# Kernel tuning notes

Measured on AMD Instinct MI355X. Metric: run time of the kernel, lower is better.

The kernel has to match this reference:

```python
import jax, jax.numpy as jnp
import numpy as np

B, S, V, D = 64, 24, 50257, 300
N, E, Ln, Le = 256, 1024, 4, 4
HL = 512               # LSTM hidden size
HEADS, HD = 4, 128
OUT = HEADS * HD       # 512, GAT out dim (concat heads)
NA = 3000              # num answers


def setup_inputs() -> dict:
    key = jax.random.key(0)
    ks = jax.random.split(key, 24)
    s = 0.02
    inp = {}
    inp["question"] = jax.random.randint(ks[0], (B, S), 0, V)
    inp["question_mask"] = jnp.ones((B, S), dtype=jnp.int32)
    inp["node_tokens"] = jax.random.randint(ks[1], (B, N, Ln), 0, V)
    inp["edge_tokens"] = jax.random.randint(ks[2], (B, E, Le), 0, V)
    inp["src_ids"] = jax.random.randint(ks[3], (B, E), 0, N)
    inp["dst_ids"] = jax.random.randint(ks[4], (B, E), 0, N)
    inp["word_emb"] = jax.random.normal(ks[5], (V, D)) * s
    inp["W_ih"] = jax.random.normal(ks[6], (D, 4 * HL)) * s
    inp["W_hh"] = jax.random.normal(ks[7], (HL, 4 * HL)) * s
    inp["b_lstm"] = jnp.zeros((4 * HL,))
    inp["W_node"] = jax.random.normal(ks[8], (D, HEADS * HD)) * s
    inp["W_rel"] = jax.random.normal(ks[9], (D, HEADS * HD)) * s
    inp["a_src"] = jax.random.normal(ks[10], (HEADS, HD)) * s
    inp["a_dst"] = jax.random.normal(ks[11], (HEADS, HD)) * s
    inp["a_edge"] = jax.random.normal(ks[12], (HEADS, HD)) * s
    inp["W_edge_upd"] = jax.random.normal(ks[13], (D, D)) * s
    inp["W_qnode"] = jax.random.normal(ks[14], (HL, OUT)) * s
    inp["b_qnode"] = jnp.zeros((OUT,))
    inp["W_qedge"] = jax.random.normal(ks[15], (HL, D)) * s
    inp["b_qedge"] = jnp.zeros((D,))
    inp["W_edge_prj"] = jax.random.normal(ks[16], (D, OUT)) * s
    inp["b_edge_prj"] = jnp.zeros((OUT,))
    inp["W_mid"] = jax.random.normal(ks[17], (2 * OUT, 3 * OUT)) * s
    inp["b_mid"] = jnp.zeros((3 * OUT,))
    inp["W_pre"] = jax.random.normal(ks[18], (3 * OUT, NA)) * s
    inp["b_pre"] = jnp.zeros((NA,))
    return inp


def _lstm_last_hidden(x, mask, W_ih, W_hh, b):
    # x: [B,S,D], mask: [B,S] -> last valid hidden state [B,HL]
    h0 = jnp.zeros((x.shape[0], HL), x.dtype)
    def step(carry, t):
        h, c = carry
        xt, mt = t
        g = xt @ W_ih + h @ W_hh + b
        i, f, gg, o = jnp.split(g, 4, axis=-1)
        c_new = jax.nn.sigmoid(f) * c + jax.nn.sigmoid(i) * jnp.tanh(gg)
        h_new = jax.nn.sigmoid(o) * jnp.tanh(c_new)
        m = (mt > 0)[:, None]
        return (jnp.where(m, h_new, h), jnp.where(m, c_new, c)), None
    (h, _), _ = jax.lax.scan(step, (h0, h0), (x.transpose(1, 0, 2), mask.T))
    return h


def reference(question, question_mask, node_tokens, edge_tokens, src_ids, dst_ids,
              word_emb, W_ih, W_hh, b_lstm, W_node, W_rel, a_src, a_dst, a_edge,
              W_edge_upd, W_qnode, b_qnode, W_qedge, b_qedge, W_edge_prj, b_edge_prj,
              W_mid, b_mid, W_pre, b_pre):
    # language encoder
    seq = word_emb[question]                               # [B,S,D]
    q_emb = _lstm_last_hidden(seq, question_mask, W_ih, W_hh, b_lstm)  # [B,HL]
    # graph features: sum word embeddings of node/edge phrases (get_graph_feat)
    nf = word_emb[node_tokens].sum(2).reshape(B * N, D)    # [BN,D]
    ef = word_emb[edge_tokens].sum(2).reshape(B * E, D)    # [BE,D]
    # batched graph with global node ids
    offs = (jnp.arange(B) * N)[:, None]
    src = (src_ids + offs).reshape(-1)
    dst = (dst_ids + offs).reshape(-1)
    # multi-head GAT with edge (relation) features
    h = (nf @ W_node).reshape(B * N, HEADS, HD)
    r = (ef @ W_rel).reshape(B * E, HEADS, HD)
    logits = jax.nn.leaky_relu(
        (h[src] * a_src).sum(-1) + (h[dst] * a_dst).sum(-1) + (r * a_edge).sum(-1),
        negative_slope=0.2)                                # [BE,HEADS]
    mx = jax.ops.segment_max(logits, dst, num_segments=B * N)
    ex = jnp.exp(logits - mx[dst])
    den = jax.ops.segment_sum(ex, dst, num_segments=B * N)
    alpha = ex / (den[dst] + 1e-9)
    node_out = jax.ops.segment_sum(alpha[..., None] * (h[src] + r), dst,
                                   num_segments=B * N)
    node_out = jax.nn.elu(node_out).reshape(B, N, OUT)     # ndata['feat']
    edge_out = jax.nn.relu(ef @ W_edge_upd).reshape(B, E, D)  # edata['feat']
    # per-graph readout (dgl.unbatch + torch.sum loop == segment sum over graphs)
    nodes = node_out.sum(1)                                # [B,OUT]
    edges = edge_out.sum(1)                                # [B,D]
    # question projections + fusion
    question_edges = (q_emb @ W_qedge + b_qedge) + edges
    question_nodes = (q_emb @ W_qnode + b_qnode) + nodes
    q_edges = question_edges @ W_edge_prj + b_edge_prj
    q = jnp.concatenate([q_edges, question_nodes], axis=1)  # [B,2*OUT]
    mid = q @ W_mid + b_mid
    return mid @ W_pre + b_pre                              # [B,NA]
```

## Files before the change

### kernel.cpp

```cpp
#include <hip/hip_runtime.h>
#include <hip/hip_bf16.h>
#include <cstdint>
#include <cstddef>

typedef unsigned short u16;
typedef __attribute__((ext_vector_type(8))) short bf16x8;
typedef __attribute__((ext_vector_type(4))) float f32x4;

#define BB   64
#define SS   24
#define DD   300
#define DP   304
#define HLS  512
#define BNN  16384
#define BEE  65536
#define NAA  3000

static constexpr size_t O_COUNTS = 0;
static constexpr size_t O_FILL   = 65536;
static constexpr size_t O_ESUM   = 131072;
static constexpr size_t O_H0     = 207872;
static constexpr size_t O_C      = 338944;
static constexpr size_t Z_BYTES  = 470016;
static constexpr size_t O_H1     = 470016;
static constexpr size_t O_XPROJ  = 601088;
static constexpr size_t O_BT_NODE = O_XPROJ;
static constexpr size_t O_BT_REL  = O_XPROJ + 311296;
static constexpr size_t O_BT_EDGE = O_XPROJ + 622592;
static constexpr size_t O_NF     = 13184000;
static constexpr size_t O_EF     = 23145472;
static constexpr size_t O_HFEAT  = 62991360;
static constexpr size_t O_RFEAT  = 79768576;
static constexpr size_t O_SSRC   = 146877440;
static constexpr size_t O_SDST   = 147139584;
static constexpr size_t O_SE     = 147401728;
static constexpr size_t O_SG     = 148450304;
static constexpr size_t O_DG     = 148712448;
static constexpr size_t O_RS     = 148974592;
static constexpr size_t O_ELIST  = 149040128;
static constexpr size_t O_LG     = 149302272;
static constexpr size_t O_NOUT   = 150350848;
static constexpr size_t O_NSUM   = 167128064;
static constexpr size_t O_QN     = 167259136;
static constexpr size_t O_QE     = 167390208;
static constexpr size_t O_QCAT   = 167467008;
static constexpr size_t O_MID    = 167729152;

__device__ __forceinline__ float bf(u16 u) {
  union { unsigned int i; float f; } c; c.i = ((unsigned int)u) << 16; return c.f;
}
__device__ __forceinline__ u16 f2bu(float f) {
  union { float f; unsigned int i; } c; c.f = f;
  unsigned int r = c.i + 0x7fffu + ((c.i >> 16) & 1u);
  return (u16)(r >> 16);
}

__global__ __launch_bounds__(256) void k_zero(float* __restrict__ p, int n) {
  int i = blockIdx.x * 256 + threadIdx.x, st = gridDim.x * 256;
  for (; i < n; i += st) p[i] = 0.f;
}

__global__ __launch_bounds__(256) void k_binit(const float* __restrict__ bias,
    const float* __restrict__ extra, float* __restrict__ out, int N, int ldo, int lde) {
  int col = blockIdx.x * 256 + threadIdx.x;
  int b = blockIdx.y;
  if (col < N) {
    float v = bias ? bias[col] : 0.f;
    if (extra) v += extra[(size_t)b * lde + col];
    out[(size_t)b * ldo + col] = v;
  }
}

__global__ __launch_bounds__(256) void k_feat(const int* __restrict__ toks, const float* __restrict__ emb,
                                              u16* __restrict__ outp) {
  int tid = threadIdx.x;
  int r = blockIdx.x * 4 + (tid >> 6);
  int lane = tid & 63;
  int t0 = toks[r * 4 + 0], t1 = toks[r * 4 + 1], t2 = toks[r * 4 + 2], t3 = toks[r * 4 + 3];
  const float* e0 = emb + (size_t)t0 * DD;
  const float* e1 = emb + (size_t)t1 * DD;
  const float* e2 = emb + (size_t)t2 * DD;
  const float* e3 = emb + (size_t)t3 * DD;
#pragma unroll
  for (int p = 0; p < 2; ++p) {
    int c = p * 256 + lane * 4;
    if (c >= DP) continue;
    ushort4 o;
    if (c + 3 < DD) {
      float4 a = *(const float4*)&e0[c], b4 = *(const float4*)&e1[c];
      float4 d = *(const float4*)&e2[c], e = *(const float4*)&e3[c];
      o.x = f2bu(a.x + b4.x + d.x + e.x);
      o.y = f2bu(a.y + b4.y + d.y + e.y);
      o.z = f2bu(a.z + b4.z + d.z + e.z);
      o.w = f2bu(a.w + b4.w + d.w + e.w);
    } else {
      o.x = o.y = o.z = o.w = 0;
    }
    *(ushort4*)&outp[(size_t)r * DP + c] = o;
  }
}

__global__ __launch_bounds__(256) void k_trans(const float* __restrict__ W, int N, int Npad,
                                               u16* __restrict__ Wt) {
  __shared__ float t[32][33];
  int tx = threadIdx.x & 31;
  int ty = threadIdx.x >> 5;
  int c0 = blockIdx.x * 32;
  int k0 = blockIdx.y * 32;
#pragma unroll
  for (int r = 0; r < 4; ++r) {
    int k = k0 + ty + r * 8;
    int c = c0 + tx;
    t[ty + r * 8][tx] = (k < DD && c < N) ? W[(size_t)k * N + c] : 0.f;
  }
  __syncthreads();
#pragma unroll
  for (int r = 0; r < 4; ++r) {
    int c = c0 + ty + r * 8;
    int k = k0 + tx;
    if (c < Npad && k < DP) Wt[(size_t)c * DP + k] = f2bu(t[tx][ty + r * 8]);
  }
}

__global__ __launch_bounds__(256) void gemm_f32(
    const float* __restrict__ A, int lda, const int* __restrict__ rowmap,
    const float* __restrict__ W, int N, int K, float* __restrict__ Cf) {
  __shared__ float As[32][128];
  __shared__ float Ws[32][128];
  int tid = threadIdx.x;
  int tx = tid & 15, ty = tid >> 4;
  int row0 = blockIdx.y * 128, col0 = blockIdx.x * 128;
  float acc[8][8];
#pragma unroll
  for (int i = 0; i < 8; ++i)
#pragma unroll
    for (int j = 0; j < 8; ++j) acc[i][j] = 0.f;
  for (int k0 = 0; k0 < K; k0 += 32) {
    for (int s = tid; s < 1024; s += 256) {
      int r = s >> 3, kc = (s & 7) << 2, kk = k0 + kc;
      float4 v = {0.f, 0.f, 0.f, 0.f};
      if (kk + 3 < K) {
        int ar = row0 + r;
        if (rowmap) ar = rowmap[ar];
        v = *(const float4*)&A[(size_t)ar * lda + kk];
      } else if (kk < K) {
        int ar = row0 + r;
        if (rowmap) ar = rowmap[ar];
        v.x = A[(size_t)ar * lda + kk];
        if (kk + 1 < K) v.y = A[(size_t)ar * lda + kk + 1];
        if (kk + 2 < K) v.z = A[(size_t)ar * lda + kk + 2];
      }
      As[kc + 0][r] = v.x; As[kc + 1][r] = v.y; As[kc + 2][r] = v.z; As[kc + 3][r] = v.w;
    }
    for (int s = tid; s < 1024; s += 256) {
      int kr = s >> 5, nc = (s & 31) << 2, kk = k0 + kr, col = col0 + nc;
      float4 wv = {0.f, 0.f, 0.f, 0.f};
      if (kk < K && col + 3 < N) wv = *(const float4*)&W[(size_t)kk * N + col];
      *(float4*)&Ws[kr][nc] = wv;
    }
    __syncthreads();
#pragma unroll 8
    for (int k = 0; k < 32; ++k) {
      float a[8], b[8];
      *(float4*)&a[0] = *(float4*)&As[k][ty * 8];
      *(float4*)&a[4] = *(float4*)&As[k][ty * 8 + 4];
      *(float4*)&b[0] = *(float4*)&Ws[k][tx * 8];
      *(float4*)&b[4] = *(float4*)&Ws[k][tx * 8 + 4];
#pragma unroll
      for (int i = 0; i < 8; ++i)
#pragma unroll
        for (int j = 0; j < 8; ++j) acc[i][j] = fmaf(a[i], b[j], acc[i][j]);
    }
    __syncthreads();
  }
#pragma unroll
  for (int i = 0; i < 8; ++i) {
    int gr = row0 + ty * 8 + i;
#pragma unroll
    for (int j = 0; j < 8; ++j) {
      int gc = col0 + tx * 8 + j;
      if (gc < N) Cf[(size_t)gr * N + gc] = acc[i][j];
    }
  }
}

__global__ __launch_bounds__(256) void gemm_mfma(
    const u16* __restrict__ A, const u16* __restrict__ Bt, int N,
    u16* __restrict__ Cb, float* __restrict__ bsum, int mode) {
  __shared__ __align__(16) u16 As[128][40];
  __shared__ __align__(16) u16 Bs[128][40];
  int tid = threadIdx.x;
  int wave = tid >> 6, lane = tid & 63;
  int wr = wave >> 1, wc = wave & 1;
  int row0 = blockIdx.y * 128, col0 = blockIdx.x * 128;
  f32x4 acc[4][4];
#pragma unroll
  for (int i = 0; i < 4; ++i)
#pragma unroll
    for (int j = 0; j < 4; ++j) acc[i][j] = (f32x4){0.f, 0.f, 0.f, 0.f};

  for (int k0 = 0; k0 < DP; k0 += 32) {
    for (int s = tid; s < 1024; s += 256) {
      int r = s >> 3, kc = (s & 7) << 2, kk = k0 + kc;
      ushort4 va = {0, 0, 0, 0}, vb = {0, 0, 0, 0};
      if (kk < DP) {
        va = *(const ushort4*)&A[(size_t)(row0 + r) * DP + kk];
        vb = *(const ushort4*)&Bt[(size_t)(col0 + r) * DP + kk];
      }
      *(ushort4*)&As[r][kc] = va;
      *(ushort4*)&Bs[r][kc] = vb;
    }
    __syncthreads();
    bf16x8 af[4], bfr[4];
    int kb = (lane >> 4) * 8;
    int rl = lane & 15;
#pragma unroll
    for (int i = 0; i < 4; ++i) {
      af[i]  = *(const bf16x8*)&As[wr * 64 + i * 16 + rl][kb];
      bfr[i] = *(const bf16x8*)&Bs[wc * 64 + i * 16 + rl][kb];
    }
#pragma unroll
    for (int i = 0; i < 4; ++i)
#pragma unroll
      for (int j = 0; j < 4; ++j)
        acc[i][j] = __builtin_amdgcn_mfma_f32_16x16x32_bf16(af[i], bfr[j], acc[i][j], 0, 0, 0);
    __syncthreads();
  }

  int g = lane >> 4, rl = lane & 15;
  if (mode == 0) {
#pragma unroll
    for (int i = 0; i < 4; ++i)
#pragma unroll
      for (int j = 0; j < 4; ++j) {
        int gc = col0 + wc * 64 + j * 16 + rl;
#pragma unroll
        for (int reg = 0; reg < 4; ++reg) {
          int gr = row0 + wr * 64 + i * 16 + g * 4 + reg;
          if (gc < N) Cb[(size_t)gr * N + gc] = f2bu(acc[i][j][reg]);
        }
      }
  } else {
    float* red = (float*)&As[0][0];
    __syncthreads();
#pragma unroll
    for (int j = 0; j < 4; ++j) {
      float s = 0.f;
#pragma unroll
      for (int i = 0; i < 4; ++i)
#pragma unroll
        for (int reg = 0; reg < 4; ++reg) s += fmaxf(acc[i][j][reg], 0.f);
      red[(wr * 4 + g) * 128 + wc * 64 + j * 16 + rl] = s;
    }
    __syncthreads();
    if (tid < 128) {
      float s = 0.f;
#pragma unroll
      for (int y = 0; y < 8; ++y) s += red[y * 128 + tid];
      int gc = col0 + tid;
      if (gc < N) atomicAdd(&bsum[(size_t)(row0 >> 10) * N + gc], s);
    }
  }
}

__global__ __launch_bounds__(256) void gemm_small(
    const float* __restrict__ A, int lda, const float* __restrict__ W,
    int N, int K, int ldo, float* __restrict__ out) {
  __shared__ float As[64][256];
  int tid = threadIdx.x;
  int k0 = blockIdx.y * 256;
  int kt = min(256, K - k0);
  int col = blockIdx.x * 64 + (tid & 63);
  int bg = tid >> 6;
  int nseg = kt >> 2;
  for (int s = tid; s < 64 * nseg; s += 256) {
    int r = s / nseg, kq = s - r * nseg;
    *(float4*)&As[r][kq << 2] = *(const float4*)&A[(size_t)r * lda + k0 + (kq << 2)];
  }
  __syncthreads();
  float acc[16];
#pragma unroll
  for (int i = 0; i < 16; ++i) acc[i] = 0.f;
  if (col < N) {
    for (int k = 0; k < kt; k += 4) {
      float w0 = W[(size_t)(k0 + k) * N + col];
      float w1 = W[(size_t)(k0 + k + 1) * N + col];
      float w2 = W[(size_t)(k0 + k + 2) * N + col];
      float w3 = W[(size_t)(k0 + k + 3) * N + col];
#pragma unroll
      for (int bi = 0; bi < 16; ++bi) {
        float4 a4 = *(const float4*)&As[bg * 16 + bi][k];
        acc[bi] = fmaf(a4.x, w0, fmaf(a4.y, w1, fmaf(a4.z, w2, fmaf(a4.w, w3, acc[bi]))));
      }
    }
#pragma unroll
    for (int bi = 0; bi < 16; ++bi)
      atomicAdd(&out[(size_t)(bg * 16 + bi) * ldo + col], acc[bi]);
  }
}

__global__ __launch_bounds__(256) void k_lstm(
    const float* __restrict__ whh, const float* __restrict__ xproj,
    const float* __restrict__ bls, const int* __restrict__ qmask,
    const float* __restrict__ h_in, float* __restrict__ h_out, float* __restrict__ c, int t) {
  __shared__ float hs[4][512];
  int tid = threadIdx.x;
  int j = (blockIdx.x << 6) + (tid & 63);
  int bq = tid >> 6;
  int b = (blockIdx.y << 2) + bq;
  for (int i = tid; i < 2048; i += 256)
    hs[i >> 9][i & 511] = h_in[(size_t)((blockIdx.y << 2) + (i >> 9)) * 512 + (i & 511)];
  __syncthreads();
  float a0 = 0.f, a1 = 0.f, a2 = 0.f, a3 = 0.f;
#pragma unroll 8
  for (int k = 0; k < 512; ++k) {
    float hv = hs[bq][k];
    const float* w = whh + (size_t)k * 2048 + j;
    a0 = fmaf(hv, w[0], a0);
    a1 = fmaf(hv, w[512], a1);
    a2 = fmaf(hv, w[1024], a2);
    a3 = fmaf(hv, w[1536], a3);
  }
  size_t xb = ((size_t)b * SS + t) * 2048;
  float gi = a0 + xproj[xb + j] + bls[j];
  float gf = a1 + xproj[xb + 512 + j] + bls[512 + j];
  float gg = a2 + xproj[xb + 1024 + j] + bls[1024 + j];
  float go = a3 + xproj[xb + 1536 + j] + bls[1536 + j];
  float si = 1.f / (1.f + __expf(-gi));
  float sf = 1.f / (1.f + __expf(-gf));
  float so = 1.f / (1.f + __expf(-go));
  float tg = 2.f / (1.f + __expf(-2.f * gg)) - 1.f;
  int idx = b * 512 + j;
  float cold = c[idx];
  float cn = sf * cold + si * tg;
  float hn = so * (2.f / (1.f + __expf(-2.f * cn)) - 1.f);
  if (qmask[b * SS + t] > 0) { c[idx] = cn; h_out[idx] = hn; }
  else h_out[idx] = h_in[idx];
}

__global__ __launch_bounds__(256) void k_snode(const u16* __restrict__ hfeat,
    const float* __restrict__ a_src, const float* __restrict__ a_dst,
    float* __restrict__ ssrc, float* __restrict__ sdst) {
  __shared__ float as[4 * 132], ad[4 * 132];
  int tid = threadIdx.x;
  for (int i = tid; i < 512; i += 256) {
    int h = i >> 7, d = i & 127;
    as[h * 132 + d] = a_src[i];
    ad[h * 132 + d] = a_dst[i];
  }
  __syncthreads();
  int id = blockIdx.x * 256 + tid;
  int n = id >> 2, h = id & 3;
  const u16* hp = hfeat + (size_t)n * 512 + h * 128;
  float s1 = 0.f, s2 = 0.f;
  for (int d = 0; d < 128; d += 4) {
    ushort4 v = *(const ushort4*)&hp[d];
    float f0 = bf(v.x), f1 = bf(v.y), f2 = bf(v.z), f3 = bf(v.w);
    int o = h * 132 + d;
    s1 += f0 * as[o] + f1 * as[o + 1] + f2 * as[o + 2] + f3 * as[o + 3];
    s2 += f0 * ad[o] + f1 * ad[o + 1] + f2 * ad[o + 2] + f3 * ad[o + 3];
  }
  ssrc[id] = s1; sdst[id] = s2;
}

__global__ __launch_bounds__(256) void k_sedge(const u16* __restrict__ rfeat,
    const float* __restrict__ a_edge, float* __restrict__ se) {
  __shared__ float ae[4 * 132];
  int tid = threadIdx.x;
  for (int i = tid; i < 512; i += 256) { int h = i >> 7, d = i & 127; ae[h * 132 + d] = a_edge[i]; }
  __syncthreads();
  int id = blockIdx.x * 256 + tid;
  int e = id >> 2, h = id & 3;
  const u16* rp = rfeat + (size_t)e * 512 + h * 128;
  float s = 0.f;
  for (int d = 0; d < 128; d += 4) {
    ushort4 v = *(const ushort4*)&rp[d];
    int o = h * 132 + d;
    s += bf(v.x) * ae[o] + bf(v.y) * ae[o + 1] + bf(v.z) * ae[o + 2] + bf(v.w) * ae[o + 3];
  }
  se[id] = s;
}

__global__ __launch_bounds__(256) void k_prep(const int* __restrict__ src, const int* __restrict__ dst,
    int* __restrict__ sg, int* __restrict__ dg, int* __restrict__ counts) {
  int i = blockIdx.x * 256 + threadIdx.x;
  int b = i >> 10;
  sg[i] = (b << 8) + src[i];
  int dgl = (b << 8) + dst[i];
  dg[i] = dgl;
  atomicAdd(&counts[dgl], 1);
}

__global__ __launch_bounds__(256) void k_scan(const int* __restrict__ counts, int* __restrict__ rs) {
  __shared__ int sc[256];
  int b = blockIdx.x, tid = threadIdx.x;
  int v = counts[b * 256 + tid];
  sc[tid] = v;
  __syncthreads();
  for (int off = 1; off < 256; off <<= 1) {
    int add = (tid >= off) ? sc[tid - off] : 0;
    __syncthreads();
    sc[tid] += add;
    __syncthreads();
  }
  rs[b * 256 + tid] = b * 1024 + sc[tid] - v;
}

__global__ __launch_bounds__(256) void k_scatter(const int* __restrict__ dg, const int* __restrict__ rs,
    int* __restrict__ fill, int* __restrict__ elist) {
  int i = blockIdx.x * 256 + threadIdx.x;
  int d = dg[i];
  int pos = rs[d] + atomicAdd(&fill[d], 1);
  elist[pos] = i;
}

__global__ __launch_bounds__(256) void k_logit(const int* __restrict__ sg, const int* __restrict__ dg,
    const float* __restrict__ ssrc, const float* __restrict__ sdst,
    const float* __restrict__ se, float* __restrict__ lg) {
  int i = blockIdx.x * 256 + threadIdx.x;
  int e = i >> 2, h = i & 3;
  float x = ssrc[sg[e] * 4 + h] + sdst[dg[e] * 4 + h] + se[i];
  lg[i] = x > 0.f ? x : 0.2f * x;
}

__global__ __launch_bounds__(256) void k_soft(const int* __restrict__ counts, const int* __restrict__ rs,
    const int* __restrict__ elist, float* __restrict__ lg) {
  int id = blockIdx.x * 256 + threadIdx.x;
  int n = id >> 2, h = id & 3;
  int deg = counts[n];
  if (deg == 0) return;
  int st = rs[n];
  float m = -1e30f;
  for (int i = 0; i < deg; ++i) { int e = elist[st + i]; m = fmaxf(m, lg[e * 4 + h]); }
  float s = 0.f;
  for (int i = 0; i < deg; ++i) {
    int e = elist[st + i];
    float p = __expf(lg[e * 4 + h] - m);
    lg[e * 4 + h] = p;
    s += p;
  }
  float inv = 1.f / (s + 1e-9f);
  for (int i = 0; i < deg; ++i) { int e = elist[st + i]; lg[e * 4 + h] *= inv; }
}

__global__ __launch_bounds__(256) void k_agg(const int* __restrict__ counts, const int* __restrict__ rs,
    const int* __restrict__ elist, const int* __restrict__ sg, const float* __restrict__ lg,
    const u16* __restrict__ hfeat, const u16* __restrict__ rfeat, u16* __restrict__ nout) {
  int n = blockIdx.x;
  int deg = counts[n], st = rs[n];
  int c1 = threadIdx.x, c2 = threadIdx.x + 256;
  float a1 = 0.f, a2 = 0.f;
  for (int i = 0; i < deg; ++i) {
    int e = elist[st + i];
    int s = sg[e];
    float al1 = lg[e * 4 + (c1 >> 7)], al2 = lg[e * 4 + (c2 >> 7)];
    a1 += al1 * (bf(hfeat[(size_t)s * 512 + c1]) + bf(rfeat[(size_t)e * 512 + c1]));
    a2 += al2 * (bf(hfeat[(size_t)s * 512 + c2]) + bf(rfeat[(size_t)e * 512 + c2]));
  }
  a1 = a1 > 0.f ? a1 : __expf(a1) - 1.f;
  a2 = a2 > 0.f ? a2 : __expf(a2) - 1.f;
  nout[(size_t)n * 512 + c1] = f2bu(a1);
  nout[(size_t)n * 512 + c2] = f2bu(a2);
}

__global__ __launch_bounds__(512) void k_nodesum(const u16* __restrict__ nout, float* __restrict__ nsum) {
  int b = blockIdx.x, col = threadIdx.x;
  float s = 0.f;
  for (int n = 0; n < 256; ++n) s += bf(nout[(size_t)((b << 8) + n) * 512 + col]);
  nsum[b * 512 + col] = s;
}

extern "C" void kernel_launch(void* const* d_in, const int* in_sizes, int n_in,
                              void* d_out, int out_size, void* d_ws, size_t ws_size,
                              hipStream_t stream) {
  const int*   question   = (const int*)d_in[0];
  const int*   qmask      = (const int*)d_in[1];
  const int*   node_toks  = (const int*)d_in[2];
  const int*   edge_toks  = (const int*)d_in[3];
  const int*   src_ids    = (const int*)d_in[4];
  const int*   dst_ids    = (const int*)d_in[5];
  const float* word_emb   = (const float*)d_in[6];
  const float* W_ih       = (const float*)d_in[7];
  const float* W_hh       = (const float*)d_in[8];
  const float* b_lstm     = (const float*)d_in[9];
  const float* W_node     = (const float*)d_in[10];
  const float* W_rel      = (const float*)d_in[11];
  const float* a_src      = (const float*)d_in[12];
  const float* a_dst      = (const float*)d_in[13];
  const float* a_edge     = (const float*)d_in[14];
  const float* W_edge_upd = (const float*)d_in[15];
  const float* W_qnode    = (const float*)d_in[16];
  const float* b_qnode    = (const float*)d_in[17];
  const float* W_qedge    = (const float*)d_in[18];
  const float* b_qedge    = (const float*)d_in[19];
  const float* W_edge_prj = (const float*)d_in[20];
  const float* b_edge_prj = (const float*)d_in[21];
  const float* W_mid      = (const float*)d_in[22];
  const float* b_mid      = (const float*)d_in[23];
  const float* W_pre      = (const float*)d_in[24];
  const float* b_pre      = (const float*)d_in[25];
  float* outp = (float*)d_out;

  char* ws = (char*)d_ws;
  int*   counts = (int*)(ws + O_COUNTS);
  int*   fill   = (int*)(ws + O_FILL);
  float* esum   = (float*)(ws + O_ESUM);
  float* h0     = (float*)(ws + O_H0);
  float* cst    = (float*)(ws + O_C);
  float* h1     = (float*)(ws + O_H1);
  float* xproj  = (float*)(ws + O_XPROJ);
  u16*   btn    = (u16*)(ws + O_BT_NODE);
  u16*   btr    = (u16*)(ws + O_BT_REL);
  u16*   bte    = (u16*)(ws + O_BT_EDGE);
  u16*   nf     = (u16*)(ws + O_NF);
  u16*   ef     = (u16*)(ws + O_EF);
  u16*   hfeat  = (u16*)(ws + O_HFEAT);
  u16*   rfeat  = (u16*)(ws + O_RFEAT);
  float* ssrc   = (float*)(ws + O_SSRC);
  float* sdst   = (float*)(ws + O_SDST);
  float* se     = (float*)(ws + O_SE);
  int*   sg     = (int*)(ws + O_SG);
  int*   dg     = (int*)(ws + O_DG);
  int*   rs     = (int*)(ws + O_RS);
  int*   elist  = (int*)(ws + O_ELIST);
  float* lg     = (float*)(ws + O_LG);
  u16*   nout   = (u16*)(ws + O_NOUT);
  float* nsum   = (float*)(ws + O_NSUM);
  float* qn     = (float*)(ws + O_QN);
  float* qe     = (float*)(ws + O_QE);
  float* qcat   = (float*)(ws + O_QCAT);
  float* midb   = (float*)(ws + O_MID);

  k_zero<<<128, 256, 0, stream>>>((float*)ws, (int)(Z_BYTES / 4));
  k_feat<<<BNN / 4, 256, 0, stream>>>(node_toks, word_emb, nf);
  k_feat<<<BEE / 4, 256, 0, stream>>>(edge_toks, word_emb, ef);
  gemm_f32<<<dim3(16, 12), 256, 0, stream>>>(word_emb, DD, question, W_ih, 2048, DD, xproj);
  for (int t = 0; t < SS; ++t) {
    const float* hin = (t & 1) ? h1 : h0;
    float* hout = (t & 1) ? h0 : h1;
    k_lstm<<<dim3(8, 16), 256, 0, stream>>>(W_hh, xproj, b_lstm, qmask, hin, hout, cst, t);
  }
  k_trans<<<dim3(16, 10), 256, 0, stream>>>(W_node, 512, 512, btn);
  k_trans<<<dim3(16, 10), 256, 0, stream>>>(W_rel, 512, 512, btr);
  k_trans<<<dim3(12, 10), 256, 0, stream>>>(W_edge_upd, 300, 384, bte);
  gemm_mfma<<<dim3(4, 128), 256, 0, stream>>>(nf, btn, 512, hfeat, nullptr, 0);
  gemm_mfma<<<dim3(4, 512), 256, 0, stream>>>(ef, btr, 512, rfeat, nullptr, 0);
  gemm_mfma<<<dim3(3, 512), 256, 0, stream>>>(ef, bte, 300, nullptr, esum, 1);
  k_snode<<<256, 256, 0, stream>>>(hfeat, a_src, a_dst, ssrc, sdst);
  k_sedge<<<1024, 256, 0, stream>>>(rfeat, a_edge, se);
  k_prep<<<256, 256, 0, stream>>>(src_ids, dst_ids, sg, dg, counts);
  k_scan<<<64, 256, 0, stream>>>(counts, rs);
  k_scatter<<<256, 256, 0, stream>>>(dg, rs, fill, elist);
  k_logit<<<1024, 256, 0, stream>>>(sg, dg, ssrc, sdst, se, lg);
  k_soft<<<256, 256, 0, stream>>>(counts, rs, elist, lg);
  k_agg<<<BNN, 256, 0, stream>>>(counts, rs, elist, sg, lg, hfeat, rfeat, nout);
  k_nodesum<<<64, 512, 0, stream>>>(nout, nsum);
  k_binit<<<dim3(2, 64), 256, 0, stream>>>(b_qnode, nsum, qn, 512, 512, 512);
  k_binit<<<dim3(2, 64), 256, 0, stream>>>(b_qedge, esum, qe, 300, 300, 300);
  gemm_small<<<dim3(8, 2), 256, 0, stream>>>(h0, 512, W_qnode, 512, 512, 512, qn);
  gemm_small<<<dim3(5, 2), 256, 0, stream>>>(h0, 512, W_qedge, 300, 512, 300, qe);
  k_binit<<<dim3(2, 64), 256, 0, stream>>>(b_edge_prj, nullptr, qcat, 512, 1024, 0);
  k_binit<<<dim3(2, 64), 256, 0, stream>>>(nullptr, qn, qcat + 512, 512, 1024, 512);
  gemm_small<<<dim3(8, 2), 256, 0, stream>>>(qe, 300, W_edge_prj, 512, 300, 1024, qcat);
  k_binit<<<dim3(6, 64), 256, 0, stream>>>(b_mid, nullptr, midb, 1536, 1536, 0);
  gemm_small<<<dim3(24, 4), 256, 0, stream>>>(qcat, 1024, W_mid, 1536, 1024, 1536, midb);
  k_binit<<<dim3(12, 64), 256, 0, stream>>>(b_pre, nullptr, outp, NAA, NAA, 0);
  gemm_small<<<dim3(47, 6), 256, 0, stream>>>(midb, 1536, W_pre, NAA, 1536, NAA, outp);
}
```

Before: 1.427 ms.

## Gate-interleave LSTM weights and fuse relation/edge GEMMs with edge attention scores

W_hh is repacked once so each LSTM step loads all four gate weights for a hidden unit as one float4. The input projection is written in the same interleaved gate order, so it can also be read as a float4. The relation-feature GEMM and the edge-update GEMM are merged into one kernel: each block loops over seven column tiles of the same edge rows, reusing the A tiles. Its epilogue computes the per-head edge attention scores, which removes the separate k_sedge pass over rfeat. This relies on the transposed edge-update weights sitting contiguously after the relation weights, and it serialises more work per block across fewer blocks.

```diff
diff --git a/kernel.cpp b/kernel.cpp
--- a/kernel.cpp
+++ b/kernel.cpp
@@ -122,9 +122,20 @@
   }
 }
 
+__global__ __launch_bounds__(256) void k_packW(const float* __restrict__ W, float* __restrict__ Wp) {
+  int idx = blockIdx.x * 256 + threadIdx.x;
+  int k = idx >> 9, j = idx & 511;
+  float4 v;
+  v.x = W[(size_t)k * 2048 + j];
+  v.y = W[(size_t)k * 2048 + 512 + j];
+  v.z = W[(size_t)k * 2048 + 1024 + j];
+  v.w = W[(size_t)k * 2048 + 1536 + j];
+  *(float4*)&Wp[(size_t)k * 2048 + j * 4] = v;
+}
+
 __global__ __launch_bounds__(256) void gemm_f32(
     const float* __restrict__ A, int lda, const int* __restrict__ rowmap,
-    const float* __restrict__ W, int N, int K, float* __restrict__ Cf) {
+    const float* __restrict__ W, int N, int K, float* __restrict__ Cf, int gatepack) {
   __shared__ float As[32][128];
   __shared__ float Ws[32][128];
   int tid = threadIdx.x;
@@ -179,14 +190,18 @@
 #pragma unroll
     for (int j = 0; j < 8; ++j) {
       int gc = col0 + tx * 8 + j;
-      if (gc < N) Cf[(size_t)gr * N + gc] = acc[i][j];
+      if (gc < N) {
+        size_t oi = gatepack ? ((size_t)gr * 2048 + ((gc & 511) << 2) + (gc >> 9))
+                             : ((size_t)gr * N + gc);
+        Cf[oi] = acc[i][j];
+      }
     }
   }
 }
 
 __global__ __launch_bounds__(256) void gemm_mfma(
-    const u16* __restrict__ A, const u16* __restrict__ Bt, int N,
-    u16* __restrict__ Cb, float* __restrict__ bsum, int mode) {
+    const u16* __restrict__ A, const u16* __restrict__ Bt,
+    u16* __restrict__ Cb, int N) {
   __shared__ __align__(16) u16 As[128][40];
   __shared__ __align__(16) u16 Bs[128][40];
   int tid = threadIdx.x;
@@ -228,37 +243,129 @@
   }
 
   int g = lane >> 4, rl = lane & 15;
-  if (mode == 0) {
+#pragma unroll
+  for (int i = 0; i < 4; ++i)
+#pragma unroll
+    for (int j = 0; j < 4; ++j) {
+      int gc = col0 + wc * 64 + j * 16 + rl;
+#pragma unroll
+      for (int reg = 0; reg < 4; ++reg) {
+        int gr = row0 + wr * 64 + i * 16 + g * 4 + reg;
+        Cb[(size_t)gr * N + gc] = f2bu(acc[i][j][reg]);
+      }
+    }
+}
+
+__global__ __launch_bounds__(256) void gemm_mfma2(
+    const u16* __restrict__ A, const u16* __restrict__ Bt,
+    u16* __restrict__ Cb, const float* __restrict__ aedge,
+    float* __restrict__ se, float* __restrict__ bsum) {
+  __shared__ __align__(16) u16 As[128][40];
+  __shared__ __align__(16) u16 Bs[128][40];
+  __shared__ float sered[2][128];
+  int tid = threadIdx.x;
+  int wave = tid >> 6, lane = tid & 63;
+  int wr = wave >> 1, wc = wave & 1;
+  int row0 = blockIdx.x * 128;
+  int g = lane >> 4, rl = lane & 15;
+  int kb = g * 8;
+
+  for (int ct = 0; ct < 7; ++ct) {
+    int col0 = ct * 128;
+    f32x4 acc[4][4];
 #pragma unroll
     for (int i = 0; i < 4; ++i)
 #pragma unroll
+      for (int j = 0; j < 4; ++j) acc[i][j] = (f32x4){0.f, 0.f, 0.f, 0.f};
+
+    for (int k0 = 0; k0 < DP; k0 += 32) {
+      for (int s = tid; s < 1024; s += 256) {
+        int r = s >> 3, kc = (s & 7) << 2, kk = k0 + kc;
+        ushort4 va = {0, 0, 0, 0}, vb = {0, 0, 0, 0};
+        if (kk < DP) {
+          va = *(const ushort4*)&A[(size_t)(row0 + r) * DP + kk];
+          vb = *(const ushort4*)&Bt[(size_t)(col0 + r) * DP + kk];
+        }
+        *(ushort4*)&As[r][kc] = va;
+        *(ushort4*)&Bs[r][kc] = vb;
+      }
+      __syncthreads();
+      bf16x8 af[4], bfr[4];
+#pragma unroll
+      for (int i = 0; i < 4; ++i) {
+        af[i]  = *(const bf16x8*)&As[wr * 64 + i * 16 + rl][kb];
+        bfr[i] = *(const bf16x8*)&Bs[wc * 64 + i * 16 + rl][kb];
+      }
+#pragma unroll
+      for (int i = 0; i < 4; ++i)
+#pragma unroll
+        for (int j = 0; j < 4; ++j)
+          acc[i][j] = __builtin_amdgcn_mfma_f32_16x16x32_bf16(af[i], bfr[j], acc[i][j], 0, 0, 0);
+      __syncthreads();
+    }
+
+    if (ct < 4) {
+#pragma unroll
+      for (int i = 0; i < 4; ++i)
+#pragma unroll
+        for (int j = 0; j < 4; ++j) {
+          int gc = col0 + wc * 64 + j * 16 + rl;
+#pragma unroll
+          for (int reg = 0; reg < 4; ++reg) {
+            int gr = row0 + wr * 64 + i * 16 + g * 4 + reg;
+            Cb[(size_t)gr * 512 + gc] = f2bu(acc[i][j][reg]);
+          }
+        }
+      float ce[4];
+#pragma unroll
+      for (int j = 0; j < 4; ++j) ce[j] = aedge[col0 + wc * 64 + j * 16 + rl];
+      float p[4][4];
+#pragma unroll
+      for (int i = 0; i < 4; ++i)
+#pragma unroll
+        for (int reg = 0; reg < 4; ++reg) {
+          float s = 0.f;
+#pragma unroll
+          for (int j = 0; j < 4; ++j) s += acc[i][j][reg] * ce[j];
+          p[i][reg] = s;
+        }
+#pragma unroll
+      for (int m = 1; m < 16; m <<= 1)
+#pragma unroll
+        for (int i = 0; i < 4; ++i)
+#pragma unroll
+          for (int reg = 0; reg < 4; ++reg)
+            p[i][reg] += __shfl_xor(p[i][reg], m);
+      if (rl == 0) {
+#pragma unroll
+        for (int i = 0; i < 4; ++i)
+#pragma unroll
+          for (int reg = 0; reg < 4; ++reg)
+            sered[wc][wr * 64 + i * 16 + g * 4 + reg] = p[i][reg];
+      }
+      __syncthreads();
+      if (tid < 128) se[(size_t)(row0 + tid) * 4 + ct] = sered[0][tid] + sered[1][tid];
+      __syncthreads();
+    } else {
+      float* red = (float*)&As[0][0];
+#pragma unroll
       for (int j = 0; j < 4; ++j) {
-        int gc = col0 + wc * 64 + j * 16 + rl;
-#pragma unroll
-        for (int reg = 0; reg < 4; ++reg) {
-          int gr = row0 + wr * 64 + i * 16 + g * 4 + reg;
-          if (gc < N) Cb[(size_t)gr * N + gc] = f2bu(acc[i][j][reg]);
-        }
-      }
-  } else {
-    float* red = (float*)&As[0][0];
-    __syncthreads();
-#pragma unroll
-    for (int j = 0; j < 4; ++j) {
-      float s = 0.f;
-#pragma unroll
-      for (int i = 0; i < 4; ++i)
-#pragma unroll
-        for (int reg = 0; reg < 4; ++reg) s += fmaxf(acc[i][j][reg], 0.f);
-      red[(wr * 4 + g) * 128 + wc * 64 + j * 16 + rl] = s;
-    }
-    __syncthreads();
-    if (tid < 128) {
-      float s = 0.f;
-#pragma unroll
-      for (int y = 0; y < 8; ++y) s += red[y * 128 + tid];
-      int gc = col0 + tid;
-      if (gc < N) atomicAdd(&bsum[(size_t)(row0 >> 10) * N + gc], s);
+        float s = 0.f;
+#pragma unroll
+        for (int i = 0; i < 4; ++i)
+#pragma unroll
+          for (int reg = 0; reg < 4; ++reg) s += fmaxf(acc[i][j][reg], 0.f);
+        red[(wr * 4 + g) * 128 + wc * 64 + j * 16 + rl] = s;
+      }
+      __syncthreads();
+      if (tid < 128) {
+        float s = 0.f;
+#pragma unroll
+        for (int y = 0; y < 8; ++y) s += red[y * 128 + tid];
+        int c = col0 - 512 + tid;
+        if (c < 300) atomicAdd(&bsum[(size_t)(row0 >> 10) * 300 + c], s);
+      }
+      __syncthreads();
     }
   }
 }
@@ -299,8 +406,8 @@
   }
 }
 
-__global__ __launch_bounds__(256) void k_lstm(
-    const float* __restrict__ whh, const float* __restrict__ xproj,
+__global__ __launch_bounds__(256) void k_lstm2(
+    const float* __restrict__ Wp, const float* __restrict__ xproj,
     const float* __restrict__ bls, const int* __restrict__ qmask,
     const float* __restrict__ h_in, float* __restrict__ h_out, float* __restrict__ c, int t) {
   __shared__ float hs[4][512];
@@ -315,17 +422,18 @@
 #pragma unroll 8
   for (int k = 0; k < 512; ++k) {
     float hv = hs[bq][k];
-    const float* w = whh + (size_t)k * 2048 + j;
-    a0 = fmaf(hv, w[0], a0);
-    a1 = fmaf(hv, w[512], a1);
-    a2 = fmaf(hv, w[1024], a2);
-    a3 = fmaf(hv, w[1536], a3);
+    float4 w = *(const float4*)&Wp[(size_t)k * 2048 + j * 4];
+    a0 = fmaf(hv, w.x, a0);
+    a1 = fmaf(hv, w.y, a1);
+    a2 = fmaf(hv, w.z, a2);
+    a3 = fmaf(hv, w.w, a3);
   }
   size_t xb = ((size_t)b * SS + t) * 2048;
-  float gi = a0 + xproj[xb + j] + bls[j];
-  float gf = a1 + xproj[xb + 512 + j] + bls[512 + j];
-  float gg = a2 + xproj[xb + 1024 + j] + bls[1024 + j];
-  float go = a3 + xproj[xb + 1536 + j] + bls[1536 + j];
+  float4 xp = *(const float4*)&xproj[xb + j * 4];
+  float gi = a0 + xp.x + bls[j];
+  float gf = a1 + xp.y + bls[512 + j];
+  float gg = a2 + xp.z + bls[1024 + j];
+  float go = a3 + xp.w + bls[1536 + j];
   float si = 1.f / (1.f + __expf(-gi));
   float sf = 1.f / (1.f + __expf(-gf));
   float so = 1.f / (1.f + __expf(-go));
@@ -361,24 +469,6 @@
     s2 += f0 * ad[o] + f1 * ad[o + 1] + f2 * ad[o + 2] + f3 * ad[o + 3];
   }
   ssrc[id] = s1; sdst[id] = s2;
-}
-
-__global__ __launch_bounds__(256) void k_sedge(const u16* __restrict__ rfeat,
-    const float* __restrict__ a_edge, float* __restrict__ se) {
-  __shared__ float ae[4 * 132];
-  int tid = threadIdx.x;
-  for (int i = tid; i < 512; i += 256) { int h = i >> 7, d = i & 127; ae[h * 132 + d] = a_edge[i]; }
-  __syncthreads();
-  int id = blockIdx.x * 256 + tid;
-  int e = id >> 2, h = id & 3;
-  const u16* rp = rfeat + (size_t)e * 512 + h * 128;
-  float s = 0.f;
-  for (int d = 0; d < 128; d += 4) {
-    ushort4 v = *(const ushort4*)&rp[d];
-    int o = h * 132 + d;
-    s += bf(v.x) * ae[o] + bf(v.y) * ae[o + 1] + bf(v.z) * ae[o + 2] + bf(v.w) * ae[o + 3];
-  }
-  se[id] = s;
 }
 
 __global__ __launch_bounds__(256) void k_prep(const int* __restrict__ src, const int* __restrict__ dst,
@@ -516,6 +606,7 @@
   u16*   ef     = (u16*)(ws + O_EF);
   u16*   hfeat  = (u16*)(ws + O_HFEAT);
   u16*   rfeat  = (u16*)(ws + O_RFEAT);
+  float* Wp     = (float*)(ws + O_RFEAT);
   float* ssrc   = (float*)(ws + O_SSRC);
   float* sdst   = (float*)(ws + O_SDST);
   float* se     = (float*)(ws + O_SE);
@@ -534,20 +625,19 @@
   k_zero<<<128, 256, 0, stream>>>((float*)ws, (int)(Z_BYTES / 4));
   k_feat<<<BNN / 4, 256, 0, stream>>>(node_toks, word_emb, nf);
   k_feat<<<BEE / 4, 256, 0, stream>>>(edge_toks, word_emb, ef);
-  gemm_f32<<<dim3(16, 12), 256, 0, stream>>>(word_emb, DD, question, W_ih, 2048, DD, xproj);
+  k_packW<<<1024, 256, 0, stream>>>(W_hh, Wp);
+  gemm_f32<<<dim3(16, 12), 256, 0, stream>>>(word_emb, DD, question, W_ih, 2048, DD, xproj, 1);
   for (int t = 0; t < SS; ++t) {
     const float* hin = (t & 1) ? h1 : h0;
     float* hout = (t & 1) ? h0 : h1;
-    k_lstm<<<dim3(8, 16), 256, 0, stream>>>(W_hh, xproj, b_lstm, qmask, hin, hout, cst, t);
+    k_lstm2<<<dim3(8, 16), 256, 0, stream>>>(Wp, xproj, b_lstm, qmask, hin, hout, cst, t);
   }
   k_trans<<<dim3(16, 10), 256, 0, stream>>>(W_node, 512, 512, btn);
   k_trans<<<dim3(16, 10), 256, 0, stream>>>(W_rel, 512, 512, btr);
   k_trans<<<dim3(12, 10), 256, 0, stream>>>(W_edge_upd, 300, 384, bte);
-  gemm_mfma<<<dim3(4, 128), 256, 0, stream>>>(nf, btn, 512, hfeat, nullptr, 0);
-  gemm_mfma<<<dim3(4, 512), 256, 0, stream>>>(ef, btr, 512, rfeat, nullptr, 0);
-  gemm_mfma<<<dim3(3, 512), 256, 0, stream>>>(ef, bte, 300, nullptr, esum, 1);
+  gemm_mfma<<<dim3(4, 128), 256, 0, stream>>>(nf, btn, hfeat, 512);
+  gemm_mfma2<<<512, 256, 0, stream>>>(ef, btr, rfeat, a_edge, se, esum);
   k_snode<<<256, 256, 0, stream>>>(hfeat, a_src, a_dst, ssrc, sdst);
-  k_sedge<<<1024, 256, 0, stream>>>(rfeat, a_edge, se);
   k_prep<<<256, 256, 0, stream>>>(src_ids, dst_ids, sg, dg, counts);
   k_scan<<<64, 256, 0, stream>>>(counts, rs);
   k_scatter<<<256, 256, 0, stream>>>(dg, rs, fill, elist);
```

New measurement: 1.229 ms. 13.9% less time.
